# Optimization experiments

Measured on AMD Instinct MI355X. Metric: run time of the kernel, lower is better.

The kernel has to match this reference:

```python
import jax, jax.numpy as jnp
import numpy as np
from jax import lax

S = 1024   # max_num_segments
CB = 25    # color_hist_bins
TB = 10    # texture_hist_bins
EPS = 1e-12


def setup_inputs() -> dict:
    key = jax.random.key(0)
    k1, k2, k3, k4 = jax.random.split(key, 4)
    B, C, R, H, W = 8, 3, 8, 512, 512
    img = jax.random.normal(k1, (B, C, H, W), jnp.float32)
    imgs_bins = jax.random.randint(k2, (B, C, H, W), 0, CB, jnp.int32)
    grads_bins = jax.random.randint(k3, (B, C, R, H, W), 0, TB, jnp.int32)
    reg_lab = jax.random.randint(k4, (B, H, W), 0, S, jnp.int32)
    return {"img": img, "imgs_bins": imgs_bins, "grads_bins": grads_bins, "reg_lab": reg_lab}


def reference(img, imgs_bins, grads_bins, reg_lab):
    B, C, H, W = img.shape
    R = grads_bins.shape[2]
    HW = H * W
    lab = reg_lab.astype(jnp.int32)

    # ---- area_per_segment: scatter_add of ones over flattened labels ----
    flat = (lab.reshape(B, HW) + (jnp.arange(B, dtype=jnp.int32) * S)[:, None]).reshape(-1)
    area = jnp.zeros(B * S, jnp.int32).at[flat].add(1).reshape(B, S)

    # ---- bbox_per_segment: scatter amin/amax of pixel coordinates ----
    yy, xx = jnp.meshgrid(jnp.arange(H, dtype=jnp.int32),
                          jnp.arange(W, dtype=jnp.int32), indexing='ij')
    xb = jnp.broadcast_to(xx.reshape(HW), (B, HW)).reshape(-1)
    yb = jnp.broadcast_to(yy.reshape(HW), (B, HW)).reshape(-1)
    xmin = jnp.full(B * S, W, jnp.int32).at[flat].min(xb)
    ymin = jnp.full(B * S, H, jnp.int32).at[flat].min(yb)
    xmax = jnp.zeros(B * S, jnp.int32).at[flat].max(xb)
    ymax = jnp.zeros(B * S, jnp.int32).at[flat].max(yb)
    # torch does xywh[2:] -= xywh[:2] (no +1), so w = xmax - xmin
    bbox_xywh = jnp.stack([xmin, ymin, xmax - xmin, ymax - ymin], -1).reshape(B, S, 4)

    area_f = area.astype(jnp.float32)

    # ---- color histogram: scatter_add of ones into [B,C,S*CB] ----
    ci = (lab[:, None, :, :] * CB + imgs_bins).reshape(B * C, HW)
    ci = (ci + (jnp.arange(B * C, dtype=jnp.int32) * (S * CB))[:, None]).reshape(-1)
    color_hist = jnp.zeros(B * C * S * CB, jnp.float32).at[ci].add(1.0).reshape(B, C, S, CB)
    color_hist = color_hist.transpose(0, 2, 1, 3).reshape(B, S, C * CB)  # [B,S,C*CB]
    color_hist = color_hist / (area_f * float(C) + EPS)[..., None]

    # ---- texture histogram: scatter_add of ones into [B,C,R,S*TB] ----
    ti = (lab[:, None, None, :, :] * TB + grads_bins).reshape(B * C * R, HW)
    ti = (ti + (jnp.arange(B * C * R, dtype=jnp.int32) * (S * TB))[:, None]).reshape(-1)
    texture_hist = jnp.zeros(B * C * R * S * TB, jnp.float32).at[ti].add(1.0).reshape(B, C, R, S, TB)
    texture_hist = texture_hist.transpose(0, 3, 1, 2, 4).reshape(B, S, C * R * TB)  # [B,S,C*R*TB]
    texture_hist = texture_hist / (area_f * float(C * R) + EPS)[..., None]

    # ---- image_scharr_gradients: depthwise-style conv2d, padding=1 ----
    sx = jnp.array([[-3., 0., 3.], [-10., 0., 10.], [-3., 0., 3.]], jnp.float32)
    kern = jnp.stack([sx, sx.T])[:, None]  # [2,1,3,3]
    grads = lax.conv_general_dilated(img.reshape(B * C, 1, H, W), kern, (1, 1), 'SAME',
                                     dimension_numbers=('NCHW', 'OIHW', 'NCHW'))
    grads = grads.reshape(B, C, 2, H, W)

    return area, bbox_xywh, color_hist, texture_hist, grads
```

## Files before the change

### kernel.cpp

```cpp
#include <hip/hip_runtime.h>

#define B_ 8
#define C_ 3
#define R_ 8
#define H_ 512
#define W_ 512
#define HW_ (H_*W_)
#define S_ 1024
#define CB_ 25
#define TB_ 10

#define O_AREA 0
#define O_BBOX 8192
#define O_COLOR 40960
#define O_TEX 655360
#define O_GRADS 2621440

#define NBBOX 8
#define NTEX (B_*C_*R_)
#define NCOL (B_*C_)
#define NHIST (NBBOX + NTEX + NCOL)
#define NCONV 1024
#define NGRID (NHIST + NCONV)

__global__ __launch_bounds__(1024) void k_fused(
    const float* __restrict__ img,
    const int* __restrict__ imgs_bins,
    const int* __restrict__ grads_bins,
    const int* __restrict__ lab,
    float* __restrict__ out) {
  __shared__ unsigned smem[12800];
  const int bid = blockIdx.x;
  const int tid = threadIdx.x;

  if (bid < NBBOX) {
    const int b = bid;
    int* mn = (int*)smem;
    for (int i = tid; i < S_; i += 1024) {
      mn[i] = W_; mn[S_ + i] = H_; mn[2*S_ + i] = 0; mn[3*S_ + i] = 0;
    }
    __syncthreads();
    const int4* lp = (const int4*)(lab + (size_t)b * HW_);
    for (int t = tid; t < HW_/4; t += 1024) {
      const int4 lv = lp[t];
      const int p = t * 4;
      const int y = p >> 9;
      const int x = p & (W_ - 1);
      atomicMin(&mn[lv.x], x);       atomicMin(&mn[S_ + lv.x], y);
      atomicMax(&mn[2*S_ + lv.x], x);   atomicMax(&mn[3*S_ + lv.x], y);
      atomicMin(&mn[lv.y], x + 1);   atomicMin(&mn[S_ + lv.y], y);
      atomicMax(&mn[2*S_ + lv.y], x + 1); atomicMax(&mn[3*S_ + lv.y], y);
      atomicMin(&mn[lv.z], x + 2);   atomicMin(&mn[S_ + lv.z], y);
      atomicMax(&mn[2*S_ + lv.z], x + 2); atomicMax(&mn[3*S_ + lv.z], y);
      atomicMin(&mn[lv.w], x + 3);   atomicMin(&mn[S_ + lv.w], y);
      atomicMax(&mn[2*S_ + lv.w], x + 3); atomicMax(&mn[3*S_ + lv.w], y);
    }
    __syncthreads();
    {
      const int xmn = mn[tid], ymn = mn[S_ + tid];
      const int xmx = mn[2*S_ + tid], ymx = mn[3*S_ + tid];
      float4 v;
      v.x = (float)xmn; v.y = (float)ymn;
      v.z = (float)(xmx - xmn); v.w = (float)(ymx - ymn);
      ((float4*)(out + O_BBOX))[b * S_ + tid] = v;
    }
  } else if (bid < NBBOX + NTEX) {
    const int plane = bid - NBBOX;
    const int b = plane / (C_*R_);
    const int cr = plane - b * (C_*R_);
    int* h = (int*)smem;
    for (int i = tid; i < S_*TB_; i += 1024) h[i] = 0;
    __syncthreads();
    const int4* bp = (const int4*)(grads_bins + (size_t)plane * HW_);
    const int4* lp = (const int4*)(lab + (size_t)b * HW_);
    for (int t = tid; t < HW_/4; t += 1024) {
      const int4 bn = bp[t];
      const int4 lv = lp[t];
      atomicAdd(&h[lv.x*TB_ + bn.x], 1);
      atomicAdd(&h[lv.y*TB_ + bn.y], 1);
      atomicAdd(&h[lv.z*TB_ + bn.z], 1);
      atomicAdd(&h[lv.w*TB_ + bn.w], 1);
    }
    __syncthreads();
    {
      const int base = tid * TB_;
      int s = 0;
      #pragma unroll
      for (int t = 0; t < TB_; ++t) s += h[base + t];
      const float inv = 1.0f / ((float)s * 24.0f + 1e-12f);
      float* o = out + O_TEX + (size_t)b * (S_ * C_*R_*TB_) + tid * (C_*R_*TB_) + cr * TB_;
      #pragma unroll
      for (int t = 0; t < TB_; ++t) o[t] = (float)h[base + t] * inv;
      if (cr == 0) out[O_AREA + b * S_ + tid] = (float)s;
    }
  } else if (bid < NHIST) {
    const int plane = bid - NBBOX - NTEX;
    const int b = plane / C_;
    const int c = plane - b * C_;
    unsigned* h = smem;
    for (int i = tid; i < (S_*CB_)/2; i += 1024) h[i] = 0;
    __syncthreads();
    const int4* bp = (const int4*)(imgs_bins + (size_t)plane * HW_);
    const int4* lp = (const int4*)(lab + (size_t)b * HW_);
    for (int t = tid; t < HW_/4; t += 1024) {
      const int4 bn = bp[t];
      const int4 lv = lp[t];
      const int j0 = lv.x*CB_ + bn.x;
      const int j1 = lv.y*CB_ + bn.y;
      const int j2 = lv.z*CB_ + bn.z;
      const int j3 = lv.w*CB_ + bn.w;
      atomicAdd(&h[j0 >> 1], 1u << ((j0 & 1) << 4));
      atomicAdd(&h[j1 >> 1], 1u << ((j1 & 1) << 4));
      atomicAdd(&h[j2 >> 1], 1u << ((j2 & 1) << 4));
      atomicAdd(&h[j3 >> 1], 1u << ((j3 & 1) << 4));
    }
    __syncthreads();
    {
      int s = 0;
      #pragma unroll
      for (int ci = 0; ci < CB_; ++ci) {
        const int j = tid * CB_ + ci;
        s += (int)((h[j >> 1] >> ((j & 1) << 4)) & 0xFFFFu);
      }
      const float inv = 1.0f / ((float)s * 3.0f + 1e-12f);
      float* o = out + O_COLOR + (size_t)b * (S_ * C_*CB_) + tid * (C_*CB_) + c * CB_;
      #pragma unroll
      for (int ci = 0; ci < CB_; ++ci) {
        const int j = tid * CB_ + ci;
        o[ci] = (float)((h[j >> 1] >> ((j & 1) << 4)) & 0xFFFFu) * inv;
      }
    }
  } else {
    const int cb = bid - NHIST;
    const int tot = B_*C_*HW_;
    for (int i = cb * 1024 + tid; i < tot; i += NCONV * 1024) {
      const int pix = i & (HW_ - 1);
      const int bc = i >> 18;
      const int x = pix & (W_ - 1);
      const int y = pix >> 9;
      const float* im = img + (size_t)bc * HW_;
      const bool xm = x > 0, xp = x < W_ - 1, ym = y > 0, yp = y < H_ - 1;
      const float i00 = (ym && xm) ? im[pix - W_ - 1] : 0.f;
      const float i01 = ym ? im[pix - W_] : 0.f;
      const float i02 = (ym && xp) ? im[pix - W_ + 1] : 0.f;
      const float i10 = xm ? im[pix - 1] : 0.f;
      const float i12 = xp ? im[pix + 1] : 0.f;
      const float i20 = (yp && xm) ? im[pix + W_ - 1] : 0.f;
      const float i21 = yp ? im[pix + W_] : 0.f;
      const float i22 = (yp && xp) ? im[pix + W_ + 1] : 0.f;
      const float gx = 3.f*(i02 - i00) + 10.f*(i12 - i10) + 3.f*(i22 - i20);
      const float gy = 3.f*(i20 - i00) + 10.f*(i21 - i01) + 3.f*(i22 - i02);
      out[O_GRADS + (size_t)(bc*2 + 0)*HW_ + pix] = gx;
      out[O_GRADS + (size_t)(bc*2 + 1)*HW_ + pix] = gy;
    }
  }
}

extern "C" void kernel_launch(void* const* d_in, const int* in_sizes, int n_in,
                              void* d_out, int out_size, void* d_ws, size_t ws_size,
                              hipStream_t stream) {
  const float* img = (const float*)d_in[0];
  const int* imgs_bins = (const int*)d_in[1];
  const int* grads_bins = (const int*)d_in[2];
  const int* reg_lab = (const int*)d_in[3];
  float* out = (float*)d_out;

  hipLaunchKernelGGL(k_fused, dim3(NGRID), dim3(1024), 0, stream,
                     img, imgs_bins, grads_bins, reg_lab, out);
}
```

Baseline: 78.12 us.

## Split bbox into partial blocks with merge pass, vectorize conv, prefetch histogram loads

The bounding-box reduction, which used to run as 8 long blocks, is split into 256 blocks that each cover a slice of one image and write packed partial min/max values to scratch. A second small kernel merges those partials, which removes the tail caused by the 8 long bbox blocks. The Scharr convolution now has each thread produce 8 pixels from register rows using float4 loads and a separable column-sum formulation. The histogram loops software-prefetch the next int4 pair. The cost is an extra kernel launch, plus a fallback that reuses the output buffer as scratch and needs a third tail kernel.

```diff
diff --git a/kernel.cpp b/kernel.cpp
--- a/kernel.cpp
+++ b/kernel.cpp
@@ -15,57 +15,96 @@
 #define O_COLOR 40960
 #define O_TEX 655360
 #define O_GRADS 2621440
-
-#define NBBOX 8
-#define NTEX (B_*C_*R_)
-#define NCOL (B_*C_)
-#define NHIST (NBBOX + NTEX + NCOL)
-#define NCONV 1024
-#define NGRID (NHIST + NCONV)
+#define OUT_TOT 15204352
+
+#define NTEX 192
+#define NCOL 24
+#define NBB  256
+#define NHIST (NTEX + NCOL + NBB)
+#define NCONV 768
+#define NGRID1 (NHIST + NCONV)
+
+#define SCR_WORDS (NBB * 2048)
+#define NEED_WS ((size_t)SCR_WORDS * 4)
+#define RID_ALL  786432
+#define RID_SAFE 753664
+
+__device__ __forceinline__ void conv_run(const float* __restrict__ img,
+                                         float* __restrict__ out, int rid) {
+  const int px0 = rid << 3;
+  const int pix0 = px0 & (HW_ - 1);
+  const int bc = px0 >> 18;
+  const int x0 = pix0 & (W_ - 1);
+  const int y = pix0 >> 9;
+  const float* im = img + (size_t)bc * HW_ + pix0;
+  const bool ym = y > 0, yp = y < H_ - 1, xm = x0 > 0, xp = x0 < W_ - 8;
+  float r0[10], r1[10], r2[10];
+  {
+    const float4 a = *(const float4*)(im);
+    const float4 c = *(const float4*)(im + 4);
+    r1[1]=a.x; r1[2]=a.y; r1[3]=a.z; r1[4]=a.w;
+    r1[5]=c.x; r1[6]=c.y; r1[7]=c.z; r1[8]=c.w;
+    r1[0] = xm ? im[-1] : 0.f;  r1[9] = xp ? im[8] : 0.f;
+  }
+  if (ym) {
+    const float* p = im - W_;
+    const float4 a = *(const float4*)(p);
+    const float4 c = *(const float4*)(p + 4);
+    r0[1]=a.x; r0[2]=a.y; r0[3]=a.z; r0[4]=a.w;
+    r0[5]=c.x; r0[6]=c.y; r0[7]=c.z; r0[8]=c.w;
+    r0[0] = xm ? p[-1] : 0.f;  r0[9] = xp ? p[8] : 0.f;
+  } else {
+    #pragma unroll
+    for (int i = 0; i < 10; ++i) r0[i] = 0.f;
+  }
+  if (yp) {
+    const float* p = im + W_;
+    const float4 a = *(const float4*)(p);
+    const float4 c = *(const float4*)(p + 4);
+    r2[1]=a.x; r2[2]=a.y; r2[3]=a.z; r2[4]=a.w;
+    r2[5]=c.x; r2[6]=c.y; r2[7]=c.z; r2[8]=c.w;
+    r2[0] = xm ? p[-1] : 0.f;  r2[9] = xp ? p[8] : 0.f;
+  } else {
+    #pragma unroll
+    for (int i = 0; i < 10; ++i) r2[i] = 0.f;
+  }
+  float cs[10], dv[10];
+  #pragma unroll
+  for (int c = 0; c < 10; ++c) {
+    cs[c] = 3.f * (r0[c] + r2[c]) + 10.f * r1[c];
+    dv[c] = r2[c] - r0[c];
+  }
+  float gx[8], gy[8];
+  #pragma unroll
+  for (int k = 0; k < 8; ++k) {
+    gx[k] = cs[k + 2] - cs[k];
+    gy[k] = 3.f * (dv[k] + dv[k + 2]) + 10.f * dv[k + 1];
+  }
+  float* og = out + O_GRADS + (size_t)(bc * 2) * HW_ + pix0;
+  *(float4*)(og)     = make_float4(gx[0], gx[1], gx[2], gx[3]);
+  *(float4*)(og + 4) = make_float4(gx[4], gx[5], gx[6], gx[7]);
+  float* oh = og + HW_;
+  *(float4*)(oh)     = make_float4(gy[0], gy[1], gy[2], gy[3]);
+  *(float4*)(oh + 4) = make_float4(gy[4], gy[5], gy[6], gy[7]);
+}
 
 __global__ __launch_bounds__(1024) void k_fused(
     const float* __restrict__ img,
     const int* __restrict__ imgs_bins,
     const int* __restrict__ grads_bins,
     const int* __restrict__ lab,
-    float* __restrict__ out) {
+    float* __restrict__ out,
+    unsigned* __restrict__ scr,
+    int ridHi) {
   __shared__ unsigned smem[12800];
   const int bid = blockIdx.x;
   const int tid = threadIdx.x;
 
-  if (bid < NBBOX) {
-    const int b = bid;
-    int* mn = (int*)smem;
-    for (int i = tid; i < S_; i += 1024) {
-      mn[i] = W_; mn[S_ + i] = H_; mn[2*S_ + i] = 0; mn[3*S_ + i] = 0;
-    }
-    __syncthreads();
-    const int4* lp = (const int4*)(lab + (size_t)b * HW_);
-    for (int t = tid; t < HW_/4; t += 1024) {
-      const int4 lv = lp[t];
-      const int p = t * 4;
-      const int y = p >> 9;
-      const int x = p & (W_ - 1);
-      atomicMin(&mn[lv.x], x);       atomicMin(&mn[S_ + lv.x], y);
-      atomicMax(&mn[2*S_ + lv.x], x);   atomicMax(&mn[3*S_ + lv.x], y);
-      atomicMin(&mn[lv.y], x + 1);   atomicMin(&mn[S_ + lv.y], y);
-      atomicMax(&mn[2*S_ + lv.y], x + 1); atomicMax(&mn[3*S_ + lv.y], y);
-      atomicMin(&mn[lv.z], x + 2);   atomicMin(&mn[S_ + lv.z], y);
-      atomicMax(&mn[2*S_ + lv.z], x + 2); atomicMax(&mn[3*S_ + lv.z], y);
-      atomicMin(&mn[lv.w], x + 3);   atomicMin(&mn[S_ + lv.w], y);
-      atomicMax(&mn[2*S_ + lv.w], x + 3); atomicMax(&mn[3*S_ + lv.w], y);
-    }
-    __syncthreads();
-    {
-      const int xmn = mn[tid], ymn = mn[S_ + tid];
-      const int xmx = mn[2*S_ + tid], ymx = mn[3*S_ + tid];
-      float4 v;
-      v.x = (float)xmn; v.y = (float)ymn;
-      v.z = (float)(xmx - xmn); v.w = (float)(ymx - ymn);
-      ((float4*)(out + O_BBOX))[b * S_ + tid] = v;
-    }
-  } else if (bid < NBBOX + NTEX) {
-    const int plane = bid - NBBOX;
+  if (bid >= NHIST) {
+    const int rid = (bid - NHIST) * 1024 + tid;
+    if (rid < ridHi) conv_run(img, out, rid);
+  } else if (bid < NTEX) {
+    const int plane = bid;
     const int b = plane / (C_*R_);
     const int cr = plane - b * (C_*R_);
     int* h = (int*)smem;
@@ -73,14 +112,21 @@
     __syncthreads();
     const int4* bp = (const int4*)(grads_bins + (size_t)plane * HW_);
     const int4* lp = (const int4*)(lab + (size_t)b * HW_);
-    for (int t = tid; t < HW_/4; t += 1024) {
-      const int4 bn = bp[t];
-      const int4 lv = lp[t];
-      atomicAdd(&h[lv.x*TB_ + bn.x], 1);
-      atomicAdd(&h[lv.y*TB_ + bn.y], 1);
-      atomicAdd(&h[lv.z*TB_ + bn.z], 1);
-      atomicAdd(&h[lv.w*TB_ + bn.w], 1);
-    }
+    int4 cb = bp[tid], cl = lp[tid];
+    #pragma unroll 1
+    for (int it = 1; it < 64; ++it) {
+      const int4 nb = bp[it * 1024 + tid];
+      const int4 nl = lp[it * 1024 + tid];
+      atomicAdd(&h[cl.x*TB_ + cb.x], 1);
+      atomicAdd(&h[cl.y*TB_ + cb.y], 1);
+      atomicAdd(&h[cl.z*TB_ + cb.z], 1);
+      atomicAdd(&h[cl.w*TB_ + cb.w], 1);
+      cb = nb; cl = nl;
+    }
+    atomicAdd(&h[cl.x*TB_ + cb.x], 1);
+    atomicAdd(&h[cl.y*TB_ + cb.y], 1);
+    atomicAdd(&h[cl.z*TB_ + cb.z], 1);
+    atomicAdd(&h[cl.w*TB_ + cb.w], 1);
     __syncthreads();
     {
       const int base = tid * TB_;
@@ -88,27 +134,40 @@
       #pragma unroll
       for (int t = 0; t < TB_; ++t) s += h[base + t];
       const float inv = 1.0f / ((float)s * 24.0f + 1e-12f);
-      float* o = out + O_TEX + (size_t)b * (S_ * C_*R_*TB_) + tid * (C_*R_*TB_) + cr * TB_;
+      float* o = out + O_TEX + (size_t)b * (S_ * 240) + tid * 240 + cr * TB_;
       #pragma unroll
       for (int t = 0; t < TB_; ++t) o[t] = (float)h[base + t] * inv;
       if (cr == 0) out[O_AREA + b * S_ + tid] = (float)s;
     }
-  } else if (bid < NHIST) {
-    const int plane = bid - NBBOX - NTEX;
+  } else if (bid < NTEX + NCOL) {
+    const int plane = bid - NTEX;
     const int b = plane / C_;
     const int c = plane - b * C_;
     unsigned* h = smem;
-    for (int i = tid; i < (S_*CB_)/2; i += 1024) h[i] = 0;
+    for (int i = tid; i < 12800; i += 1024) h[i] = 0;
     __syncthreads();
     const int4* bp = (const int4*)(imgs_bins + (size_t)plane * HW_);
     const int4* lp = (const int4*)(lab + (size_t)b * HW_);
-    for (int t = tid; t < HW_/4; t += 1024) {
-      const int4 bn = bp[t];
-      const int4 lv = lp[t];
-      const int j0 = lv.x*CB_ + bn.x;
-      const int j1 = lv.y*CB_ + bn.y;
-      const int j2 = lv.z*CB_ + bn.z;
-      const int j3 = lv.w*CB_ + bn.w;
+    int4 cb = bp[tid], cl = lp[tid];
+    #pragma unroll 1
+    for (int it = 1; it < 64; ++it) {
+      const int4 nb = bp[it * 1024 + tid];
+      const int4 nl = lp[it * 1024 + tid];
+      const int j0 = cl.x*CB_ + cb.x;
+      const int j1 = cl.y*CB_ + cb.y;
+      const int j2 = cl.z*CB_ + cb.z;
+      const int j3 = cl.w*CB_ + cb.w;
+      atomicAdd(&h[j0 >> 1], 1u << ((j0 & 1) << 4));
+      atomicAdd(&h[j1 >> 1], 1u << ((j1 & 1) << 4));
+      atomicAdd(&h[j2 >> 1], 1u << ((j2 & 1) << 4));
+      atomicAdd(&h[j3 >> 1], 1u << ((j3 & 1) << 4));
+      cb = nb; cl = nl;
+    }
+    {
+      const int j0 = cl.x*CB_ + cb.x;
+      const int j1 = cl.y*CB_ + cb.y;
+      const int j2 = cl.z*CB_ + cb.z;
+      const int j3 = cl.w*CB_ + cb.w;
       atomicAdd(&h[j0 >> 1], 1u << ((j0 & 1) << 4));
       atomicAdd(&h[j1 >> 1], 1u << ((j1 & 1) << 4));
       atomicAdd(&h[j2 >> 1], 1u << ((j2 & 1) << 4));
@@ -123,7 +182,7 @@
         s += (int)((h[j >> 1] >> ((j & 1) << 4)) & 0xFFFFu);
       }
       const float inv = 1.0f / ((float)s * 3.0f + 1e-12f);
-      float* o = out + O_COLOR + (size_t)b * (S_ * C_*CB_) + tid * (C_*CB_) + c * CB_;
+      float* o = out + O_COLOR + (size_t)b * (S_ * 75) + tid * 75 + c * CB_;
       #pragma unroll
       for (int ci = 0; ci < CB_; ++ci) {
         const int j = tid * CB_ + ci;
@@ -131,29 +190,48 @@
       }
     }
   } else {
-    const int cb = bid - NHIST;
-    const int tot = B_*C_*HW_;
-    for (int i = cb * 1024 + tid; i < tot; i += NCONV * 1024) {
-      const int pix = i & (HW_ - 1);
-      const int bc = i >> 18;
-      const int x = pix & (W_ - 1);
-      const int y = pix >> 9;
-      const float* im = img + (size_t)bc * HW_;
-      const bool xm = x > 0, xp = x < W_ - 1, ym = y > 0, yp = y < H_ - 1;
-      const float i00 = (ym && xm) ? im[pix - W_ - 1] : 0.f;
-      const float i01 = ym ? im[pix - W_] : 0.f;
-      const float i02 = (ym && xp) ? im[pix - W_ + 1] : 0.f;
-      const float i10 = xm ? im[pix - 1] : 0.f;
-      const float i12 = xp ? im[pix + 1] : 0.f;
-      const float i20 = (yp && xm) ? im[pix + W_ - 1] : 0.f;
-      const float i21 = yp ? im[pix + W_] : 0.f;
-      const float i22 = (yp && xp) ? im[pix + W_ + 1] : 0.f;
-      const float gx = 3.f*(i02 - i00) + 10.f*(i12 - i10) + 3.f*(i22 - i20);
-      const float gy = 3.f*(i20 - i00) + 10.f*(i21 - i01) + 3.f*(i22 - i02);
-      out[O_GRADS + (size_t)(bc*2 + 0)*HW_ + pix] = gx;
-      out[O_GRADS + (size_t)(bc*2 + 1)*HW_ + pix] = gy;
-    }
-  }
+    const int rid2 = bid - NTEX - NCOL;
+    const int b = rid2 >> 5, q = rid2 & 31;
+    int* mn = (int*)smem;
+    mn[tid] = W_; mn[1024 + tid] = H_; mn[2048 + tid] = 0; mn[3072 + tid] = 0;
+    __syncthreads();
+    const int4* lp = (const int4*)(lab + (size_t)b * HW_) + q * 2048;
+    const int4 l0 = lp[tid], l1 = lp[tid + 1024];
+    const int p0 = (q * 2048 + tid) * 4, p1 = p0 + 4096;
+    #define BB(L,P) { const int yy = (P) >> 9, xx = (P) & (W_-1); \
+      atomicMin(&mn[L], xx); atomicMin(&mn[1024 + (L)], yy); \
+      atomicMax(&mn[2048 + (L)], xx); atomicMax(&mn[3072 + (L)], yy); }
+    BB(l0.x, p0) BB(l0.y, p0+1) BB(l0.z, p0+2) BB(l0.w, p0+3)
+    BB(l1.x, p1) BB(l1.y, p1+1) BB(l1.z, p1+2) BB(l1.w, p1+3)
+    #undef BB
+    __syncthreads();
+    unsigned* dst = scr + (size_t)rid2 * 2048;
+    dst[tid]        = (unsigned)mn[tid]        | ((unsigned)mn[1024 + tid] << 16);
+    dst[1024 + tid] = (unsigned)mn[2048 + tid] | ((unsigned)mn[3072 + tid] << 16);
+  }
+}
+
+__global__ __launch_bounds__(1024) void k_bb_merge(float* __restrict__ out,
+                                                   const unsigned* __restrict__ scr) {
+  const int b = blockIdx.x, l = threadIdx.x;
+  int xmn = W_, ymn = H_, xmx = 0, ymx = 0;
+  const unsigned* p = scr + (size_t)(b * 32) * 2048 + l;
+  #pragma unroll
+  for (int k = 0; k < 32; ++k) {
+    const unsigned w0 = p[k * 2048];
+    const unsigned w1 = p[k * 2048 + 1024];
+    xmn = min(xmn, (int)(w0 & 0xFFFFu)); ymn = min(ymn, (int)(w0 >> 16));
+    xmx = max(xmx, (int)(w1 & 0xFFFFu)); ymx = max(ymx, (int)(w1 >> 16));
+  }
+  float4 v;
+  v.x = (float)xmn; v.y = (float)ymn;
+  v.z = (float)(xmx - xmn); v.w = (float)(ymx - ymn);
+  ((float4*)(out + O_BBOX))[b * S_ + l] = v;
+}
+
+__global__ __launch_bounds__(1024) void k_conv_tail(const float* __restrict__ img,
+                                                    float* __restrict__ out) {
+  conv_run(img, out, RID_SAFE + blockIdx.x * 1024 + threadIdx.x);
 }
 
 extern "C" void kernel_launch(void* const* d_in, const int* in_sizes, int n_in,
@@ -165,6 +243,15 @@
   const int* reg_lab = (const int*)d_in[3];
   float* out = (float*)d_out;
 
-  hipLaunchKernelGGL(k_fused, dim3(NGRID), dim3(1024), 0, stream,
-                     img, imgs_bins, grads_bins, reg_lab, out);
-}
+  const bool ws_ok = ws_size >= NEED_WS;
+  unsigned* scr = ws_ok ? (unsigned*)d_ws : (unsigned*)(out + (OUT_TOT - SCR_WORDS));
+  const int ridHi = ws_ok ? RID_ALL : RID_SAFE;
+
+  hipLaunchKernelGGL(k_fused, dim3(NGRID1), dim3(1024), 0, stream,
+                     img, imgs_bins, grads_bins, reg_lab, out, scr, ridHi);
+  hipLaunchKernelGGL(k_bb_merge, dim3(8), dim3(1024), 0, stream, out, scr);
+  if (!ws_ok) {
+    hipLaunchKernelGGL(k_conv_tail, dim3((RID_ALL - RID_SAFE) / 1024), dim3(1024),
+                       0, stream, img, out);
+  }
+}
```

Result: slower. 88.38 us (+13.1%).

## Pre-pack segment labels to 16-bit pairs to cut label read traffic

Applied to the files above, without the earlier changes.

Adds a pre-pass kernel that packs the int32 region labels into 16-bit pairs, stored in workspace or in a scratch tail of the output buffer. The histogram and bbox blocks then read half as many label bytes per pixel and process eight pixels per iteration. When no workspace is available, the last conv planes are computed by a separate tail kernel after the scratch region has been consumed. The aim is to reduce the heavy repeated reads of the label array across the 216 histogram planes, at the cost of an extra launch and an extra pass over the labels.

```diff
diff --git a/kernel.cpp b/kernel.cpp
--- a/kernel.cpp
+++ b/kernel.cpp
@@ -15,6 +15,7 @@
 #define O_COLOR 40960
 #define O_TEX 655360
 #define O_GRADS 2621440
+#define OUT_TOT 15204352
 
 #define NBBOX 8
 #define NTEX (B_*C_*R_)
@@ -23,12 +24,32 @@
 #define NCONV 1024
 #define NGRID (NHIST + NCONV)
 
+#define PK_WORDS 1048576
+#define NEED_WS ((size_t)PK_WORDS * 4)
+#define SCR_OFF (OUT_TOT - PK_WORDS)
+#define CONV_SAFE (22 << 18)
+#define CONV_ALL  (24 << 18)
+
+__global__ __launch_bounds__(1024) void k_pack(const int* __restrict__ lab,
+                                               unsigned* __restrict__ plab) {
+  const int i = blockIdx.x * 1024 + threadIdx.x;
+  const int4 a = ((const int4*)lab)[2 * i];
+  const int4 b = ((const int4*)lab)[2 * i + 1];
+  uint4 o;
+  o.x = (unsigned)(a.x) | ((unsigned)a.y << 16);
+  o.y = (unsigned)(a.z) | ((unsigned)a.w << 16);
+  o.z = (unsigned)(b.x) | ((unsigned)b.y << 16);
+  o.w = (unsigned)(b.z) | ((unsigned)b.w << 16);
+  ((uint4*)plab)[i] = o;
+}
+
 __global__ __launch_bounds__(1024) void k_fused(
     const float* __restrict__ img,
     const int* __restrict__ imgs_bins,
     const int* __restrict__ grads_bins,
-    const int* __restrict__ lab,
-    float* __restrict__ out) {
+    const unsigned* __restrict__ plab,
+    float* __restrict__ out,
+    int convHi) {
   __shared__ unsigned smem[12800];
   const int bid = blockIdx.x;
   const int tid = threadIdx.x;
@@ -36,24 +57,22 @@
   if (bid < NBBOX) {
     const int b = bid;
     int* mn = (int*)smem;
-    for (int i = tid; i < S_; i += 1024) {
-      mn[i] = W_; mn[S_ + i] = H_; mn[2*S_ + i] = 0; mn[3*S_ + i] = 0;
-    }
-    __syncthreads();
-    const int4* lp = (const int4*)(lab + (size_t)b * HW_);
-    for (int t = tid; t < HW_/4; t += 1024) {
-      const int4 lv = lp[t];
-      const int p = t * 4;
+    mn[tid] = W_; mn[S_ + tid] = H_; mn[2*S_ + tid] = 0; mn[3*S_ + tid] = 0;
+    __syncthreads();
+    const uint4* lp = (const uint4*)(plab + (size_t)b * (HW_/2));
+    for (int t = tid; t < HW_/8; t += 1024) {
+      const uint4 L = lp[t];
+      const int p = t * 8;
       const int y = p >> 9;
       const int x = p & (W_ - 1);
-      atomicMin(&mn[lv.x], x);       atomicMin(&mn[S_ + lv.x], y);
-      atomicMax(&mn[2*S_ + lv.x], x);   atomicMax(&mn[3*S_ + lv.x], y);
-      atomicMin(&mn[lv.y], x + 1);   atomicMin(&mn[S_ + lv.y], y);
-      atomicMax(&mn[2*S_ + lv.y], x + 1); atomicMax(&mn[3*S_ + lv.y], y);
-      atomicMin(&mn[lv.z], x + 2);   atomicMin(&mn[S_ + lv.z], y);
-      atomicMax(&mn[2*S_ + lv.z], x + 2); atomicMax(&mn[3*S_ + lv.z], y);
-      atomicMin(&mn[lv.w], x + 3);   atomicMin(&mn[S_ + lv.w], y);
-      atomicMax(&mn[2*S_ + lv.w], x + 3); atomicMax(&mn[3*S_ + lv.w], y);
+      #define BBX(l, xx) { const int ll = (int)(l); \
+        atomicMin(&mn[ll], xx);        atomicMin(&mn[S_ + ll], y); \
+        atomicMax(&mn[2*S_ + ll], xx); atomicMax(&mn[3*S_ + ll], y); }
+      BBX(L.x & 0xFFFFu, x)     BBX(L.x >> 16, x + 1)
+      BBX(L.y & 0xFFFFu, x + 2) BBX(L.y >> 16, x + 3)
+      BBX(L.z & 0xFFFFu, x + 4) BBX(L.z >> 16, x + 5)
+      BBX(L.w & 0xFFFFu, x + 6) BBX(L.w >> 16, x + 7)
+      #undef BBX
     }
     __syncthreads();
     {
@@ -72,14 +91,19 @@
     for (int i = tid; i < S_*TB_; i += 1024) h[i] = 0;
     __syncthreads();
     const int4* bp = (const int4*)(grads_bins + (size_t)plane * HW_);
-    const int4* lp = (const int4*)(lab + (size_t)b * HW_);
-    for (int t = tid; t < HW_/4; t += 1024) {
-      const int4 bn = bp[t];
-      const int4 lv = lp[t];
-      atomicAdd(&h[lv.x*TB_ + bn.x], 1);
-      atomicAdd(&h[lv.y*TB_ + bn.y], 1);
-      atomicAdd(&h[lv.z*TB_ + bn.z], 1);
-      atomicAdd(&h[lv.w*TB_ + bn.w], 1);
+    const uint4* lp = (const uint4*)(plab + (size_t)b * (HW_/2));
+    for (int t = tid; t < HW_/8; t += 1024) {
+      const uint4 L = lp[t];
+      const int4 b0 = bp[2*t];
+      const int4 b1 = bp[2*t + 1];
+      atomicAdd(&h[(int)(L.x & 0xFFFFu)*TB_ + b0.x], 1);
+      atomicAdd(&h[(int)(L.x >> 16)*TB_ + b0.y], 1);
+      atomicAdd(&h[(int)(L.y & 0xFFFFu)*TB_ + b0.z], 1);
+      atomicAdd(&h[(int)(L.y >> 16)*TB_ + b0.w], 1);
+      atomicAdd(&h[(int)(L.z & 0xFFFFu)*TB_ + b1.x], 1);
+      atomicAdd(&h[(int)(L.z >> 16)*TB_ + b1.y], 1);
+      atomicAdd(&h[(int)(L.w & 0xFFFFu)*TB_ + b1.z], 1);
+      atomicAdd(&h[(int)(L.w >> 16)*TB_ + b1.w], 1);
     }
     __syncthreads();
     {
@@ -88,7 +112,7 @@
       #pragma unroll
       for (int t = 0; t < TB_; ++t) s += h[base + t];
       const float inv = 1.0f / ((float)s * 24.0f + 1e-12f);
-      float* o = out + O_TEX + (size_t)b * (S_ * C_*R_*TB_) + tid * (C_*R_*TB_) + cr * TB_;
+      float* o = out + O_TEX + (size_t)b * (S_ * 240) + tid * 240 + cr * TB_;
       #pragma unroll
       for (int t = 0; t < TB_; ++t) o[t] = (float)h[base + t] * inv;
       if (cr == 0) out[O_AREA + b * S_ + tid] = (float)s;
@@ -101,18 +125,18 @@
     for (int i = tid; i < (S_*CB_)/2; i += 1024) h[i] = 0;
     __syncthreads();
     const int4* bp = (const int4*)(imgs_bins + (size_t)plane * HW_);
-    const int4* lp = (const int4*)(lab + (size_t)b * HW_);
-    for (int t = tid; t < HW_/4; t += 1024) {
-      const int4 bn = bp[t];
-      const int4 lv = lp[t];
-      const int j0 = lv.x*CB_ + bn.x;
-      const int j1 = lv.y*CB_ + bn.y;
-      const int j2 = lv.z*CB_ + bn.z;
-      const int j3 = lv.w*CB_ + bn.w;
-      atomicAdd(&h[j0 >> 1], 1u << ((j0 & 1) << 4));
-      atomicAdd(&h[j1 >> 1], 1u << ((j1 & 1) << 4));
-      atomicAdd(&h[j2 >> 1], 1u << ((j2 & 1) << 4));
-      atomicAdd(&h[j3 >> 1], 1u << ((j3 & 1) << 4));
+    const uint4* lp = (const uint4*)(plab + (size_t)b * (HW_/2));
+    for (int t = tid; t < HW_/8; t += 1024) {
+      const uint4 L = lp[t];
+      const int4 b0 = bp[2*t];
+      const int4 b1 = bp[2*t + 1];
+      #define CADD(l, bin) { const int j = (int)(l)*CB_ + (bin); \
+        atomicAdd(&h[j >> 1], 1u << ((j & 1) << 4)); }
+      CADD(L.x & 0xFFFFu, b0.x) CADD(L.x >> 16, b0.y)
+      CADD(L.y & 0xFFFFu, b0.z) CADD(L.y >> 16, b0.w)
+      CADD(L.z & 0xFFFFu, b1.x) CADD(L.z >> 16, b1.y)
+      CADD(L.w & 0xFFFFu, b1.z) CADD(L.w >> 16, b1.w)
+      #undef CADD
     }
     __syncthreads();
     {
@@ -123,7 +147,7 @@
         s += (int)((h[j >> 1] >> ((j & 1) << 4)) & 0xFFFFu);
       }
       const float inv = 1.0f / ((float)s * 3.0f + 1e-12f);
-      float* o = out + O_COLOR + (size_t)b * (S_ * C_*CB_) + tid * (C_*CB_) + c * CB_;
+      float* o = out + O_COLOR + (size_t)b * (S_ * 75) + tid * 75 + c * CB_;
       #pragma unroll
       for (int ci = 0; ci < CB_; ++ci) {
         const int j = tid * CB_ + ci;
@@ -132,8 +156,7 @@
     }
   } else {
     const int cb = bid - NHIST;
-    const int tot = B_*C_*HW_;
-    for (int i = cb * 1024 + tid; i < tot; i += NCONV * 1024) {
+    for (int i = cb * 1024 + tid; i < convHi; i += NCONV * 1024) {
       const int pix = i & (HW_ - 1);
       const int bc = i >> 18;
       const int x = pix & (W_ - 1);
@@ -156,6 +179,29 @@
   }
 }
 
+__global__ __launch_bounds__(1024) void k_conv_tail(const float* __restrict__ img,
+                                                    float* __restrict__ out) {
+  const int i = CONV_SAFE + blockIdx.x * 1024 + threadIdx.x;
+  const int pix = i & (HW_ - 1);
+  const int bc = i >> 18;
+  const int x = pix & (W_ - 1);
+  const int y = pix >> 9;
+  const float* im = img + (size_t)bc * HW_;
+  const bool xm = x > 0, xp = x < W_ - 1, ym = y > 0, yp = y < H_ - 1;
+  const float i00 = (ym && xm) ? im[pix - W_ - 1] : 0.f;
+  const float i01 = ym ? im[pix - W_] : 0.f;
+  const float i02 = (ym && xp) ? im[pix - W_ + 1] : 0.f;
+  const float i10 = xm ? im[pix - 1] : 0.f;
+  const float i12 = xp ? im[pix + 1] : 0.f;
+  const float i20 = (yp && xm) ? im[pix + W_ - 1] : 0.f;
+  const float i21 = yp ? im[pix + W_] : 0.f;
+  const float i22 = (yp && xp) ? im[pix + W_ + 1] : 0.f;
+  const float gx = 3.f*(i02 - i00) + 10.f*(i12 - i10) + 3.f*(i22 - i20);
+  const float gy = 3.f*(i20 - i00) + 10.f*(i21 - i01) + 3.f*(i22 - i02);
+  out[O_GRADS + (size_t)(bc*2 + 0)*HW_ + pix] = gx;
+  out[O_GRADS + (size_t)(bc*2 + 1)*HW_ + pix] = gy;
+}
+
 extern "C" void kernel_launch(void* const* d_in, const int* in_sizes, int n_in,
                               void* d_out, int out_size, void* d_ws, size_t ws_size,
                               hipStream_t stream) {
@@ -165,6 +211,14 @@
   const int* reg_lab = (const int*)d_in[3];
   float* out = (float*)d_out;
 
+  const bool ws_ok = ws_size >= NEED_WS;
+  unsigned* plab = ws_ok ? (unsigned*)d_ws : (unsigned*)(out + SCR_OFF);
+  const int convHi = ws_ok ? CONV_ALL : CONV_SAFE;
+
+  hipLaunchKernelGGL(k_pack, dim3(256), dim3(1024), 0, stream, reg_lab, plab);
   hipLaunchKernelGGL(k_fused, dim3(NGRID), dim3(1024), 0, stream,
-                     img, imgs_bins, grads_bins, reg_lab, out);
-}
+                     img, imgs_bins, grads_bins, plab, out, convHi);
+  if (!ws_ok) {
+    hipLaunchKernelGGL(k_conv_tail, dim3(512), dim3(1024), 0, stream, img, out);
+  }
+}
```

After: 78.21 us, median of 2. No clear change (+0.1%).
